# Kernel optimization log

Hardware: AMD Instinct MI355X
Metric: run time of the kernel (lower is better)

The kernel has to match this reference:

```python
import jax, jax.numpy as jnp
import numpy as np

IN_F, OUT_F, K = 1024, 1024, 12
EPS = 1e-6


def setup_inputs() -> dict:
    key = jax.random.key(0)
    k1, k2, k3, k4 = jax.random.split(key, 4)
    x = jax.random.normal(k1, (4, 4096, IN_F), dtype=jnp.float32)
    # grid: linspace(-2,2,K) per feature + small noise so sort is nontrivial
    base = jnp.linspace(-2.0, 2.0, K, dtype=jnp.float32)
    grid = base[None, :] + 0.1 * jax.random.normal(k2, (IN_F, K), dtype=jnp.float32)
    coeffs = 0.1 * jax.random.normal(k3, (IN_F, K), dtype=jnp.float32)
    tangents = jnp.zeros((IN_F, K), dtype=jnp.float32)
    knot_alive = jnp.full((IN_F, K), 3.0, dtype=jnp.float32)
    kw1, kw2 = jax.random.split(k4)
    proj_w = jax.random.normal(kw1, (OUT_F, IN_F), dtype=jnp.float32) / np.sqrt(IN_F)
    proj_b = jnp.zeros((OUT_F,), dtype=jnp.float32)
    res_w = jax.random.normal(kw2, (OUT_F, IN_F), dtype=jnp.float32) / np.sqrt(IN_F)
    return {"x": x, "grid": grid, "coeffs": coeffs, "tangents": tangents,
            "knot_alive": knot_alive, "proj_w": proj_w, "proj_b": proj_b, "res_w": res_w}


def _eval_hermite_spline(x, grid, coeffs, tangents, knot_alive):
    # sort knots per input feature (grid: [F,K])
    sort_idx = jnp.argsort(grid, axis=1)
    sorted_grid = jnp.take_along_axis(grid, sort_idx, axis=1)
    sorted_coeffs = jnp.take_along_axis(coeffs, sort_idx, axis=1)
    sorted_tangents = jnp.take_along_axis(tangents, sort_idx, axis=1)
    sorted_alive = jnp.take_along_axis(knot_alive, sort_idx, axis=1)
    alive = jax.nn.sigmoid(sorted_alive)
    mc = sorted_coeffs * alive          # masked heights [F,K]
    mt = sorted_tangents * alive        # masked tangents [F,K]

    orig_shape = x.shape
    xf = x.reshape(-1, orig_shape[-1])  # [M,F]
    gmin = sorted_grid[:, 0]            # [F]
    gmax = sorted_grid[:, -1]
    xc = jnp.clip(xf, gmin[None, :], gmax[None, :])
    grange = jnp.maximum(gmax - gmin, EPS)
    xn = (xc - gmin[None, :]) / grange[None, :] * (K - 1)  # [M,F]
    idx_l = jnp.clip(xn.astype(jnp.int32), 0, K - 2)
    t = xn - idx_l.astype(xf.dtype)

    feat = jnp.arange(xf.shape[1])[None, :]  # [1,F] broadcast against [M,F] idx
    p0 = mc[feat, idx_l]
    p1 = mc[feat, idx_l + 1]
    m0 = mt[feat, idx_l]
    m1 = mt[feat, idx_l + 1]
    x_left = sorted_grid[feat, idx_l]
    x_right = sorted_grid[feat, idx_l + 1]
    dx = jnp.maximum(x_right - x_left, EPS)

    t2 = t * t
    t3 = t2 * t
    h00 = 2 * t3 - 3 * t2 + 1
    h10 = t3 - 2 * t2 + t
    h01 = -2 * t3 + 3 * t2
    h11 = t3 - t2
    out = h00 * p0 + h10 * m0 * dx + h01 * p1 + h11 * m1 * dx
    return out.reshape(orig_shape)


def reference(x, grid, coeffs, tangents, knot_alive, proj_w, proj_b, res_w):
    spline_out = _eval_hermite_spline(x, grid, coeffs, tangents, knot_alive)
    # proj(spline_out) + residual(x); torch Linear: y = x @ W.T + b
    return (jnp.einsum('...i,oi->...o', spline_out, proj_w) + proj_b
            + jnp.einsum('...i,oi->...o', x, res_w))
```

## Files before the change

### kernel.cpp

```cpp
#include <hip/hip_runtime.h>
#include <hip/hip_bf16.h>


#define IN_F   1024
#define OUT_F  1024
#define KNOTS  12
#define M_ROWS 16384
#define GK     2048

#define BM   256
#define BN   256
#define BKT  64
#define NTK  (GK / BKT)

typedef __attribute__((ext_vector_type(8)))  __bf16 bf16x8;
typedef __attribute__((ext_vector_type(4)))  float  f32x4;
typedef __attribute__((ext_vector_type(16))) float  f32x16;

__device__ __forceinline__ unsigned short f2bf(float v) {
    unsigned int u = __float_as_uint(v);
    u = (u + 0x7fffu + ((u >> 16) & 1u)) >> 16;
    return (unsigned short)u;
}

__device__ __forceinline__ void gload16(const void* g, void* l) {
    __builtin_amdgcn_global_load_lds(
        (const __attribute__((address_space(1))) void*)g,
        (__attribute__((address_space(3))) void*)l, 16, 0, 0);
}

__global__ __launch_bounds__(256) void prep_kernel(
    const float* __restrict__ grid, const float* __restrict__ coeffs,
    const float* __restrict__ tangents, const float* __restrict__ alive,
    float* __restrict__ gmin, float* __restrict__ scale, float4* __restrict__ H)
{
    int f = blockIdx.x * blockDim.x + threadIdx.x;
    if (f >= IN_F) return;
    float g[KNOTS], c[KNOTS], t[KNOTS], a[KNOTS];
    for (int i = 0; i < KNOTS; ++i) {
        g[i] = grid[f*KNOTS+i];  c[i] = coeffs[f*KNOTS+i];
        t[i] = tangents[f*KNOTS+i]; a[i] = alive[f*KNOTS+i];
    }
    for (int i = 1; i < KNOTS; ++i) {
        float gk=g[i], ck=c[i], tk=t[i], ak=a[i];
        int j = i-1;
        while (j >= 0 && g[j] > gk) { g[j+1]=g[j]; c[j+1]=c[j]; t[j+1]=t[j]; a[j+1]=a[j]; --j; }
        g[j+1]=gk; c[j+1]=ck; t[j+1]=tk; a[j+1]=ak;
    }
    float mcl[KNOTS], mtl[KNOTS];
    for (int i = 0; i < KNOTS; ++i) {
        float s = 1.f / (1.f + expf(-a[i]));
        mcl[i] = c[i]*s;  mtl[i] = t[i]*s;
    }
    gmin[f] = g[0];
    float grange = fmaxf(g[KNOTS-1] - g[0], 1e-6f);
    scale[f] = (float)(KNOTS-1) / grange;
    for (int k = 0; k < KNOTS-1; ++k) {
        float dx = fmaxf(g[k+1]-g[k], 1e-6f);
        H[(size_t)f*KNOTS + k] = make_float4(mcl[k], mcl[k+1], mtl[k]*dx, mtl[k+1]*dx);
    }
    H[(size_t)f*KNOTS + KNOTS-1] = make_float4(0.f, 0.f, 0.f, 0.f);
}

#define SROWS 64
#define HPAD  13
__global__ __launch_bounds__(256) void spline_kernel(const float* __restrict__ x,
    const float* __restrict__ gmin, const float* __restrict__ scale,
    const float4* __restrict__ H, unsigned short* __restrict__ A)
{
    __shared__ float4 sH[256 * HPAD];
    __shared__ float  sGm[256], sSc[256];
    const int tid  = threadIdx.x;
    const int fblk = blockIdx.y * 256;
    #pragma unroll
    for (int k = 0; k < KNOTS; ++k) sH[tid*HPAD + k] = H[(size_t)(fblk+tid)*KNOTS + k];
    sGm[tid] = gmin[fblk+tid];
    sSc[tid] = scale[fblk+tid];
    __syncthreads();

    const int wave = tid >> 6, lane = tid & 63;
    const int f0 = lane * 4;
    const float4 gm4 = *reinterpret_cast<const float4*>(&sGm[f0]);
    const float4 sc4 = *reinterpret_cast<const float4*>(&sSc[f0]);
    const float gms[4] = {gm4.x, gm4.y, gm4.z, gm4.w};
    const float scs[4] = {sc4.x, sc4.y, sc4.z, sc4.w};
    const int r0 = blockIdx.x * SROWS;

    #pragma unroll 2
    for (int r = wave; r < SROWS; r += 4) {
        const int row = r0 + r;
        const float4 xv = *reinterpret_cast<const float4*>(x + (size_t)row*IN_F + fblk + f0);
        const float xs[4] = {xv.x, xv.y, xv.z, xv.w};
        ushort4 so, xo;
        unsigned short* sp = (unsigned short*)&so;
        unsigned short* xp = (unsigned short*)&xo;
        #pragma unroll
        for (int j = 0; j < 4; ++j) {
            const float xi = xs[j];
            float xn = (xi - gms[j]) * scs[j];
            xn = fminf(fmaxf(xn, 0.f), (float)(KNOTS-1));
            int idx = (int)xn;  idx = idx > (KNOTS-2) ? (KNOTS-2) : idx;
            const float tt = xn - (float)idx;
            const float4 h = sH[(f0+j)*HPAD + idx];
            const float t2 = tt*tt, t3 = t2*tt;
            const float h00 =  2.f*t3 - 3.f*t2 + 1.f;
            const float h01 = -2.f*t3 + 3.f*t2;
            const float h10 =  t3 - 2.f*t2 + tt;
            const float h11 =  t3 - t2;
            sp[j] = f2bf(h00*h.x + h01*h.y + h10*h.z + h11*h.w);
            xp[j] = f2bf(xi);
        }
        const size_t base = (size_t)row * GK + fblk + f0;
        *reinterpret_cast<ushort4*>(A + base)        = so;
        *reinterpret_cast<ushort4*>(A + base + IN_F) = xo;
    }
}

__global__ __launch_bounds__(256) void bcast_kernel(
    const float* __restrict__ P, const float* __restrict__ R,
    unsigned short* __restrict__ Bc)
{
    int g = blockIdx.x*256 + threadIdx.x;
    int n  = g >> 9;
    int k4 = (g & 511) * 4;
    const float* src = (k4 < IN_F) ? (P + (size_t)n*IN_F + k4)
                                   : (R + (size_t)n*IN_F + (k4 - IN_F));
    float4 v = *reinterpret_cast<const float4*>(src);
    ushort4 o;
    o.x = f2bf(v.x); o.y = f2bf(v.y); o.z = f2bf(v.z); o.w = f2bf(v.w);
    *reinterpret_cast<ushort4*>(Bc + (size_t)n*GK + k4) = o;
}

__global__ __launch_bounds__(512, 2) void gemm_kernel(
    const unsigned short* __restrict__ A, const unsigned short* __restrict__ B,
    const float* __restrict__ bias, float* __restrict__ C)
{
    __shared__ unsigned short sA[2][BM*BKT];
    __shared__ unsigned short sB[2][BN*BKT];

    const int tid  = threadIdx.x;
    const int wg   = blockIdx.x;
    const int swzb = (wg & 7) * 32 + (wg >> 3);
    const int by   = swzb >> 2;
    const int bx   = swzb & 3;

    const int lane = tid & 63;
    const int wave = tid >> 6;
    const int wr   = wave >> 2;
    const int wc   = wave & 3;
    const int l31  = lane & 31;
    const int hi   = lane >> 5;

    const size_t aRow0 = (size_t)by * BM;
    const size_t bRow0 = (size_t)bx * BN;

    auto stage = [&](const unsigned short* __restrict__ G, size_t gRow0,
                     unsigned short* lds, int ts) {
        const int k0 = ts * BKT;
        #pragma unroll
        for (int i = 0; i < 4; ++i) {
            const int L16  = i*512 + tid;
            const int lrow = L16 >> 3;
            const int ss   = (L16 & 7) ^ (lrow & 7);
            gload16(G + (gRow0 + lrow)*GK + k0 + ss*8, lds + (size_t)L16*8);
        }
    };
    auto rd = [&](const unsigned short* s, int row, int ks16) -> bf16x8 {
        const int sp = (ks16*2 + hi) ^ (row & 7);
        return *reinterpret_cast<const bf16x8*>(s + row*BKT + sp*8);
    };

    f32x16 acc[4][2] = {};

    stage(A, aRow0, &sA[0][0], 0);
    stage(B, bRow0, &sB[0][0], 0);

    for (int t = 0; t < NTK; ++t) {
        const int b = t & 1;
        const unsigned short* cA = &sA[b][0];
        const unsigned short* cB = &sB[b][0];

        asm volatile("s_waitcnt vmcnt(0)" ::: "memory");
        __builtin_amdgcn_s_barrier();

        {
            bf16x8 av[4][2], bv[2][2];
            #pragma unroll
            for (int m = 0; m < 4; ++m)
                #pragma unroll
                for (int s = 0; s < 2; ++s)
                    av[m][s] = rd(cA, wr*128 + m*32 + l31, s);
            #pragma unroll
            for (int n = 0; n < 2; ++n)
                #pragma unroll
                for (int s = 0; s < 2; ++s)
                    bv[n][s] = rd(cB, wc*64 + n*32 + l31, s);
            if (t + 1 < NTK) {
                stage(A, aRow0, &sA[b^1][0], t+1);
                stage(B, bRow0, &sB[b^1][0], t+1);
            }
            __builtin_amdgcn_s_setprio(1);
            #pragma unroll
            for (int m = 0; m < 4; ++m)
              #pragma unroll
              for (int n = 0; n < 2; ++n)
                #pragma unroll
                for (int s = 0; s < 2; ++s)
                    acc[m][n] = __builtin_amdgcn_mfma_f32_32x32x16_bf16(
                        av[m][s], bv[n][s], acc[m][n], 0, 0, 0);
            __builtin_amdgcn_s_setprio(0);
        }

        {
            bf16x8 av[4][2], bv[2][2];
            #pragma unroll
            for (int m = 0; m < 4; ++m)
                #pragma unroll
                for (int s = 0; s < 2; ++s)
                    av[m][s] = rd(cA, wr*128 + m*32 + l31, 2+s);
            #pragma unroll
            for (int n = 0; n < 2; ++n)
                #pragma unroll
                for (int s = 0; s < 2; ++s)
                    bv[n][s] = rd(cB, wc*64 + n*32 + l31, 2+s);
            __builtin_amdgcn_s_setprio(1);
            #pragma unroll
            for (int m = 0; m < 4; ++m)
              #pragma unroll
              for (int n = 0; n < 2; ++n)
                #pragma unroll
                for (int s = 0; s < 2; ++s)
                    acc[m][n] = __builtin_amdgcn_mfma_f32_32x32x16_bf16(
                        av[m][s], bv[n][s], acc[m][n], 0, 0, 0);
            __builtin_amdgcn_s_setprio(0);
        }
    }

    #pragma unroll
    for (int n = 0; n < 2; ++n) {
        const int col = bx*BN + wc*64 + n*32 + l31;
        const float bv = bias[col];
        #pragma unroll
        for (int m = 0; m < 4; ++m) {
            const int rowbase = by*BM + wr*128 + m*32 + 4*hi;
            #pragma unroll
            for (int q = 0; q < 4; ++q)
                #pragma unroll
                for (int r = 0; r < 4; ++r)
                    C[(size_t)(rowbase + 8*q + r)*OUT_F + col] = acc[m][n][q*4+r] + bv;
        }
    }
}

__global__ __launch_bounds__(256) void fallback_kernel(
    const float* __restrict__ x, const float* __restrict__ P,
    const float* __restrict__ R, const float* __restrict__ pb,
    const float* __restrict__ gmin, const float* __restrict__ scale,
    const float4* __restrict__ H, float* __restrict__ out)
{
    __shared__ float s_s[IN_F];
    __shared__ float s_x[IN_F];
    int row = blockIdx.x;
    const float* xr = x + (size_t)row*IN_F;
    for (int f = threadIdx.x; f < IN_F; f += 256) {
        float xi = xr[f];
        float xn = (xi - gmin[f]) * scale[f];
        xn = fminf(fmaxf(xn, 0.f), (float)(KNOTS-1));
        int idx = (int)xn;  idx = idx > (KNOTS-2) ? (KNOTS-2) : idx;
        float tt = xn - (float)idx;
        float4 h = H[(size_t)f*KNOTS + idx];
        float t2 = tt*tt, t3 = t2*tt;
        s_s[f] = (2.f*t3-3.f*t2+1.f)*h.x + (-2.f*t3+3.f*t2)*h.y
               + (t3-2.f*t2+tt)*h.z + (t3-t2)*h.w;
        s_x[f] = xi;
    }
    __syncthreads();
    for (int j = 0; j < 4; ++j) {
        int o = threadIdx.x + j*256;
        const float* Pr = P + (size_t)o*IN_F;
        const float* Rr = R + (size_t)o*IN_F;
        float acc = pb[o];
        for (int f = 0; f < IN_F; ++f)
            acc = fmaf(s_s[f], Pr[f], fmaf(s_x[f], Rr[f], acc));
        out[(size_t)row*OUT_F + o] = acc;
    }
}

extern "C" void kernel_launch(void* const* d_in, const int* in_sizes, int n_in,
                              void* d_out, int out_size, void* d_ws, size_t ws_size,
                              hipStream_t stream) {
    const float* x         = (const float*)d_in[0];
    const float* grid      = (const float*)d_in[1];
    const float* coeffs    = (const float*)d_in[2];
    const float* tangents  = (const float*)d_in[3];
    const float* knotalive = (const float*)d_in[4];
    const float* proj_w    = (const float*)d_in[5];
    const float* proj_b    = (const float*)d_in[6];
    const float* res_w     = (const float*)d_in[7];
    float* out = (float*)d_out;

    const size_t needB  = (size_t)OUT_F * GK * 2;
    const size_t needA  = (size_t)M_ROWS * GK * 2;
    const size_t needT  = ((size_t)IN_F*2 + (size_t)IN_F*KNOTS*4) * 4;

    char* ws = (char*)d_ws;
    if (ws_size >= needB + needA + needT) {
        unsigned short* Bcat = (unsigned short*)ws;
        unsigned short* Abuf = (unsigned short*)(ws + needB);
        float*  gmin = (float*)(ws + needB + needA);
        float*  scl  = gmin + IN_F;
        float4* H    = (float4*)(scl + IN_F);

        prep_kernel<<<(IN_F+255)/256, 256, 0, stream>>>(grid, coeffs, tangents, knotalive,
                                                        gmin, scl, H);
        bcast_kernel<<<(OUT_F*GK/4)/256, 256, 0, stream>>>(proj_w, res_w, Bcat);
        spline_kernel<<<dim3(M_ROWS/SROWS, IN_F/256), 256, 0, stream>>>(x, gmin, scl, H, Abuf);
        gemm_kernel<<<(M_ROWS/BM)*(OUT_F/BN), 512, 0, stream>>>(Abuf, Bcat, proj_b, out);
    } else {
        float*  gmin = (float*)ws;
        float*  scl  = gmin + IN_F;
        float4* H    = (float4*)(scl + IN_F);
        prep_kernel<<<(IN_F+255)/256, 256, 0, stream>>>(grid, coeffs, tangents, knotalive,
                                                        gmin, scl, H);
        fallback_kernel<<<M_ROWS, 256, 0, stream>>>(x, proj_w, res_w, proj_b,
                                                    gmin, scl, H, out);
    }
}
```

Baseline: 116.3 us.

## Use 16 waves per GEMM block with 16x16x32 MFMA tiles

Doubles the GEMM block to 1024 threads (16 waves in a 4x4 grid, each owning a 64x64 sub-tile) and switches from 32x32x16 to 16x16x32 bf16 MFMA, which shrinks the per-wave accumulator from 128 to 64 floats. The aim is more waves per CU to hide LDS and global latency. In exchange each wave does more LDS fragment reads per MFMA, and the launch bound of 4 blocks per CU cannot be met with about 128KB of LDS per block.

New measurement: 104.7 us. 1.11x faster.

```diff
diff --git a/kernel.cpp b/kernel.cpp
--- a/kernel.cpp
+++ b/kernel.cpp
@@ -13,9 +13,8 @@
 #define BKT  64
 #define NTK  (GK / BKT)
 
-typedef __attribute__((ext_vector_type(8)))  __bf16 bf16x8;
-typedef __attribute__((ext_vector_type(4)))  float  f32x4;
-typedef __attribute__((ext_vector_type(16))) float  f32x16;
+typedef __attribute__((ext_vector_type(8))) __bf16 bf16x8;
+typedef __attribute__((ext_vector_type(4))) float  f32x4;
 
 __device__ __forceinline__ unsigned short f2bf(float v) {
     unsigned int u = __float_as_uint(v);
@@ -131,7 +130,7 @@
     *reinterpret_cast<ushort4*>(Bc + (size_t)n*GK + k4) = o;
 }
 
-__global__ __launch_bounds__(512, 2) void gemm_kernel(
+__global__ __launch_bounds__(1024, 4) void gemm_kernel(
     const unsigned short* __restrict__ A, const unsigned short* __restrict__ B,
     const float* __restrict__ bias, float* __restrict__ C)
 {
@@ -146,10 +145,10 @@
 
     const int lane = tid & 63;
     const int wave = tid >> 6;
-    const int wr   = wave >> 2;
-    const int wc   = wave & 3;
-    const int l31  = lane & 31;
-    const int hi   = lane >> 5;
+    const int wm   = wave >> 2;
+    const int wn   = wave & 3;
+    const int lr   = lane & 15;
+    const int lsl  = lane >> 4;
 
     const size_t aRow0 = (size_t)by * BM;
     const size_t bRow0 = (size_t)bx * BN;
@@ -158,19 +157,19 @@
                      unsigned short* lds, int ts) {
         const int k0 = ts * BKT;
         #pragma unroll
-        for (int i = 0; i < 4; ++i) {
-            const int L16  = i*512 + tid;
+        for (int i = 0; i < 2; ++i) {
+            const int L16  = i*1024 + tid;
             const int lrow = L16 >> 3;
             const int ss   = (L16 & 7) ^ (lrow & 7);
             gload16(G + (gRow0 + lrow)*GK + k0 + ss*8, lds + (size_t)L16*8);
         }
     };
-    auto rd = [&](const unsigned short* s, int row, int ks16) -> bf16x8 {
-        const int sp = (ks16*2 + hi) ^ (row & 7);
-        return *reinterpret_cast<const bf16x8*>(s + row*BKT + sp*8);
+    auto rd = [&](const unsigned short* s, int lrow, int ks) -> bf16x8 {
+        const int sp = (ks*4 + lsl) ^ (lrow & 7);
+        return *reinterpret_cast<const bf16x8*>(s + lrow*BKT + sp*8);
     };
 
-    f32x16 acc[4][2] = {};
+    f32x4 acc[4][4] = {};
 
     stage(A, aRow0, &sA[0][0], 0);
     stage(B, bRow0, &sB[0][0], 0);
@@ -184,17 +183,11 @@
         __builtin_amdgcn_s_barrier();
 
         {
-            bf16x8 av[4][2], bv[2][2];
-            #pragma unroll
-            for (int m = 0; m < 4; ++m)
-                #pragma unroll
-                for (int s = 0; s < 2; ++s)
-                    av[m][s] = rd(cA, wr*128 + m*32 + l31, s);
-            #pragma unroll
-            for (int n = 0; n < 2; ++n)
-                #pragma unroll
-                for (int s = 0; s < 2; ++s)
-                    bv[n][s] = rd(cB, wc*64 + n*32 + l31, s);
+            bf16x8 av[4], bv[4];
+            #pragma unroll
+            for (int m = 0; m < 4; ++m) av[m] = rd(cA, wm*64 + m*16 + lr, 0);
+            #pragma unroll
+            for (int n = 0; n < 4; ++n) bv[n] = rd(cB, wn*64 + n*16 + lr, 0);
             if (t + 1 < NTK) {
                 stage(A, aRow0, &sA[b^1][0], t+1);
                 stage(B, bRow0, &sB[b^1][0], t+1);
@@ -203,51 +196,36 @@
             #pragma unroll
             for (int m = 0; m < 4; ++m)
               #pragma unroll
-              for (int n = 0; n < 2; ++n)
-                #pragma unroll
-                for (int s = 0; s < 2; ++s)
-                    acc[m][n] = __builtin_amdgcn_mfma_f32_32x32x16_bf16(
-                        av[m][s], bv[n][s], acc[m][n], 0, 0, 0);
+              for (int n = 0; n < 4; ++n)
+                acc[m][n] = __builtin_amdgcn_mfma_f32_16x16x32_bf16(av[m], bv[n], acc[m][n], 0, 0, 0);
             __builtin_amdgcn_s_setprio(0);
         }
-
         {
-            bf16x8 av[4][2], bv[2][2];
-            #pragma unroll
-            for (int m = 0; m < 4; ++m)
-                #pragma unroll
-                for (int s = 0; s < 2; ++s)
-                    av[m][s] = rd(cA, wr*128 + m*32 + l31, 2+s);
-            #pragma unroll
-            for (int n = 0; n < 2; ++n)
-                #pragma unroll
-                for (int s = 0; s < 2; ++s)
-                    bv[n][s] = rd(cB, wc*64 + n*32 + l31, 2+s);
+            bf16x8 av[4], bv[4];
+            #pragma unroll
+            for (int m = 0; m < 4; ++m) av[m] = rd(cA, wm*64 + m*16 + lr, 1);
+            #pragma unroll
+            for (int n = 0; n < 4; ++n) bv[n] = rd(cB, wn*64 + n*16 + lr, 1);
             __builtin_amdgcn_s_setprio(1);
             #pragma unroll
             for (int m = 0; m < 4; ++m)
               #pragma unroll
-              for (int n = 0; n < 2; ++n)
-                #pragma unroll
-                for (int s = 0; s < 2; ++s)
-                    acc[m][n] = __builtin_amdgcn_mfma_f32_32x32x16_bf16(
-                        av[m][s], bv[n][s], acc[m][n], 0, 0, 0);
+              for (int n = 0; n < 4; ++n)
+                acc[m][n] = __builtin_amdgcn_mfma_f32_16x16x32_bf16(av[m], bv[n], acc[m][n], 0, 0, 0);
             __builtin_amdgcn_s_setprio(0);
         }
     }
 
     #pragma unroll
-    for (int n = 0; n < 2; ++n) {
-        const int col = bx*BN + wc*64 + n*32 + l31;
+    for (int n = 0; n < 4; ++n) {
+        const int col = bx*BN + wn*64 + n*16 + lr;
         const float bv = bias[col];
         #pragma unroll
         for (int m = 0; m < 4; ++m) {
-            const int rowbase = by*BM + wr*128 + m*32 + 4*hi;
-            #pragma unroll
-            for (int q = 0; q < 4; ++q)
-                #pragma unroll
-                for (int r = 0; r < 4; ++r)
-                    C[(size_t)(rowbase + 8*q + r)*OUT_F + col] = acc[m][n][q*4+r] + bv;
+            const int grow = by*BM + wm*64 + m*16 + lsl*4;
+            #pragma unroll
+            for (int r = 0; r < 4; ++r)
+                C[(size_t)(grow + r)*OUT_F + col] = acc[m][n][r] + bv;
         }
     }
 }
@@ -315,7 +293,7 @@
                                                         gmin, scl, H);
         bcast_kernel<<<(OUT_F*GK/4)/256, 256, 0, stream>>>(proj_w, res_w, Bcat);
         spline_kernel<<<dim3(M_ROWS/SROWS, IN_F/256), 256, 0, stream>>>(x, gmin, scl, H, Abuf);
-        gemm_kernel<<<(M_ROWS/BM)*(OUT_F/BN), 512, 0, stream>>>(Abuf, Bcat, proj_b, out);
+        gemm_kernel<<<(M_ROWS/BM)*(OUT_F/BN), 1024, 0, stream>>>(Abuf, Bcat, proj_b, out);
     } else {
         float*  gmin = (float*)ws;
         float*  scl  = gmin + IN_F;
```
